# Optimization experiments

Hardware: AMD Instinct MI355X
Metric: run time of the kernel (lower is better)

Reference implementation:

```python
import jax, jax.numpy as jnp
import numpy as np

N, E, D, H, ED = 50000, 800000, 128, 4, 64
C = D // H  # per-head channels
EPS = 1e-5


def setup_inputs() -> dict:
    key = jax.random.key(0)
    ks = jax.random.split(key, 16)
    s = 0.05
    return {
        "x": jax.random.normal(ks[0], (N, D), jnp.float32),
        "edge_index": jax.random.randint(ks[1], (2, E), 0, N, jnp.int64 if jax.config.jax_enable_x64 else jnp.int32),
        "edge_attr": jax.random.normal(ks[2], (E, ED), jnp.float32),
        "Wq": jax.random.normal(ks[3], (D, H * C), jnp.float32) * s,
        "bq": jnp.zeros((H * C,), jnp.float32),
        "Wk": jax.random.normal(ks[4], (D, H * C), jnp.float32) * s,
        "bk": jnp.zeros((H * C,), jnp.float32),
        "Wv": jax.random.normal(ks[5], (D, H * C), jnp.float32) * s,
        "bv": jnp.zeros((H * C,), jnp.float32),
        "We": jax.random.normal(ks[6], (ED, H * C), jnp.float32) * s,  # lin_edge, bias=False
        "Wskip": jax.random.normal(ks[7], (D, H * C), jnp.float32) * s,
        "bskip": jnp.zeros((H * C,), jnp.float32),
        "Wbeta": jax.random.normal(ks[8], (3 * H * C, 1), jnp.float32) * s,  # lin_beta, bias=False
        "gamma": jnp.ones((D,), jnp.float32),
        "beta_ln": jnp.zeros((D,), jnp.float32),
    }


def _transformer_conv(x, src, dst, edge_attr, Wq, bq, Wk, bk, Wv, bv, We, Wskip, bskip, Wbeta):
    q = (x @ Wq + bq).reshape(N, H, C)
    k = (x @ Wk + bk).reshape(N, H, C)
    v = (x @ Wv + bv).reshape(N, H, C)
    e = (edge_attr @ We).reshape(E, H, C)
    k_j = k[src] + e                     # [E,H,C]
    v_j = v[src] + e                     # [E,H,C]
    alpha = jnp.einsum("ehc,ehc->eh", q[dst], k_j) / jnp.sqrt(jnp.float32(C))
    # per-destination softmax over incoming edges
    m = jax.ops.segment_max(alpha, dst, num_segments=N)          # [N,H]
    m = jnp.where(jnp.isfinite(m), m, 0.0)
    a = jnp.exp(alpha - m[dst])
    denom = jax.ops.segment_sum(a, dst, num_segments=N)          # [N,H]
    alpha = a / jnp.where(denom > 0, denom, 1.0)[dst]
    out = jax.ops.segment_sum(alpha[:, :, None] * v_j, dst, num_segments=N)  # [N,H,C]
    out = out.reshape(N, H * C)
    # beta-gated skip (beta=True, root_weight)
    x_r = x @ Wskip + bskip
    b = jax.nn.sigmoid(jnp.concatenate([out, x_r, out - x_r], axis=-1) @ Wbeta)  # [N,1]
    return b * x_r + (1.0 - b) * out


def reference(x, edge_index, edge_attr, Wq, bq, Wk, bk, Wv, bv, We, Wskip, bskip, Wbeta, gamma, beta_ln):
    src, dst = edge_index[0], edge_index[1]
    res = _transformer_conv(x, src, dst, edge_attr, Wq, bq, Wk, bk, Wv, bv, We, Wskip, bskip, Wbeta)
    out = jax.nn.gelu(res, approximate=False) + x
    mu = jnp.mean(out, axis=-1, keepdims=True)
    var = jnp.var(out, axis=-1, keepdims=True)
    return (out - mu) * jax.lax.rsqrt(var + EPS) * gamma + beta_ln
```

## Files before the change

### kernel.cpp

```cpp
#include <hip/hip_runtime.h>
#include <math.h>

#define NN 50000
#define EE 800000

typedef __bf16 bf16x8 __attribute__((ext_vector_type(8)));
typedef float f32x4 __attribute__((ext_vector_type(4)));
typedef float f32x2 __attribute__((ext_vector_type(2)));
typedef unsigned short ushort_t;
typedef unsigned int uint_t;

__device__ inline ushort_t f2bf(float f) {
  uint_t u = __float_as_uint(f);
  uint_t r = (u + 0x7fffu + ((u >> 16) & 1u)) >> 16;
  return (ushort_t)r;
}
__device__ inline float bflo(uint_t u) { return __uint_as_float(u << 16); }
__device__ inline float bfhi(uint_t u) { return __uint_as_float(u & 0xffff0000u); }

__device__ inline uint_t pk4_fp8(float a0, float a1, float a2, float a3) {
  a0 = fminf(fmaxf(a0, -448.f), 448.f);
  a1 = fminf(fmaxf(a1, -448.f), 448.f);
  a2 = fminf(fmaxf(a2, -448.f), 448.f);
  a3 = fminf(fmaxf(a3, -448.f), 448.f);
  uint_t lo = (uint_t)__builtin_amdgcn_cvt_pk_fp8_f32(a0, a1, 0, false) & 0xFFFFu;
  uint_t hi = (uint_t)__builtin_amdgcn_cvt_pk_fp8_f32(a2, a3, 0, false) & 0xFFFFu;
  return lo | (hi << 16);
}

__device__ inline void wave_sync() {
  asm volatile("s_waitcnt lgkmcnt(0)" ::: "memory");
  __builtin_amdgcn_wave_barrier();
}

__global__ __launch_bounds__(256) void k_prepA(const float* __restrict__ Wbeta,
                                               float* __restrict__ wcomb,
                                               int* __restrict__ counts) {
  int b = blockIdx.x;
  int o = threadIdx.x;
  if (b == 0) {
    if (o < 128) {
      wcomb[o]       = Wbeta[o]       + Wbeta[256 + o];
      wcomb[128 + o] = Wbeta[128 + o] - Wbeta[256 + o];
    }
  } else {
    int i = (b - 1) * 256 + o;
    if (i < NN) counts[i] = 0;
  }
}

__global__ __launch_bounds__(256) void k_prepB(
    const float* __restrict__ Wq, const float* __restrict__ Wk,
    const float* __restrict__ Wv, const float* __restrict__ Ws,
    const float* __restrict__ bq, const float* __restrict__ bk,
    const float* __restrict__ bv, const float* __restrict__ bs,
    ushort_t* __restrict__ Wbt, float* __restrict__ bcat,
    const float* __restrict__ We, ushort_t* __restrict__ WebT,
    const int* __restrict__ ei, int* __restrict__ counts) {
  int b = blockIdx.x;
  if (b >= 288) {
    int i = (b - 288) * 256 + threadIdx.x;
    if (i < EE) atomicAdd(&counts[ei[EE + i]], 1);
    return;
  }
  if (b >= 256) {
    int i = (b - 256) * 256 + threadIdx.x;
    int c = i >> 6, k = i & 63;
    WebT[c * 64 + k] = f2bf(We[k * 128 + c]);
    return;
  }
  int i = b * 256 + threadIdx.x;
  int c = i >> 7, k = i & 127;
  float w;
  if (c < 128)      w = Wq[k * 128 + c];
  else if (c < 256) w = Wk[k * 128 + (c - 128)];
  else if (c < 384) w = Wv[k * 128 + (c - 256)];
  else              w = Ws[k * 128 + (c - 384)];
  Wbt[(size_t)c * 128 + k] = f2bf(w);
  if (i < 512) {
    float bb;
    if (i < 128)      bb = bq[i];
    else if (i < 256) bb = bk[i - 128];
    else if (i < 384) bb = bv[i - 256];
    else              bb = bs[i - 384];
    bcat[i] = bb;
  }
}

__global__ __launch_bounds__(256) void k_mm(const float* __restrict__ x,
                                            const ushort_t* __restrict__ Wbt,
                                            const float* __restrict__ bcat,
                                            ushort_t* __restrict__ qb,
                                            ushort_t* __restrict__ kb,
                                            ushort_t* __restrict__ vb,
                                            ushort_t* __restrict__ xrb) {
  __shared__ ushort_t As[128 * 128];
  __shared__ ushort_t Bs[128 * 128];
  int t = threadIdx.x;
  int rb = blockIdx.x * 128;
  int cb = blockIdx.y * 128;

  for (int q = t; q < 2048; q += 256) {
    int r = q >> 4, j = q & 15;
    int row = rb + r;
    float4 f0 = make_float4(0.f, 0.f, 0.f, 0.f), f1 = f0;
    if (row < NN) {
      const float4* xp = (const float4*)&x[(size_t)row * 128 + j * 8];
      f0 = xp[0]; f1 = xp[1];
    }
    uint_t u0 = (uint_t)f2bf(f0.x) | ((uint_t)f2bf(f0.y) << 16);
    uint_t u1 = (uint_t)f2bf(f0.z) | ((uint_t)f2bf(f0.w) << 16);
    uint_t u2 = (uint_t)f2bf(f1.x) | ((uint_t)f2bf(f1.y) << 16);
    uint_t u3 = (uint_t)f2bf(f1.z) | ((uint_t)f2bf(f1.w) << 16);
    int e = r * 128 + ((j * 8) ^ ((r & 7) << 3));
    *(uint4*)&As[e] = make_uint4(u0, u1, u2, u3);
  }
  for (int q = t; q < 2048; q += 256) {
    int c = q >> 4, j = q & 15;
    uint4 w = *(const uint4*)&Wbt[(size_t)(cb + c) * 128 + j * 8];
    int e = c * 128 + ((j * 8) ^ ((c & 7) << 3));
    *(uint4*)&Bs[e] = w;
  }
  __syncthreads();

  int lane = t & 63;
  int wv = t >> 6;
  int wr = wv >> 1, wc = wv & 1;
  int l15 = lane & 15, l4 = lane >> 4;

  f32x4 acc[4][4];
#pragma unroll
  for (int i = 0; i < 4; ++i)
#pragma unroll
    for (int j = 0; j < 4; ++j) acc[i][j] = (f32x4){0.f, 0.f, 0.f, 0.f};

#pragma unroll
  for (int ks = 0; ks < 4; ++ks) {
    int kbv = ks * 32 + l4 * 8;
    bf16x8 af[4], bfr[4];
#pragma unroll
    for (int i = 0; i < 4; ++i) {
      int r = wr * 64 + i * 16 + l15;
      af[i] = *(const bf16x8*)&As[r * 128 + (kbv ^ ((r & 7) << 3))];
    }
#pragma unroll
    for (int j = 0; j < 4; ++j) {
      int c = wc * 64 + j * 16 + l15;
      bfr[j] = *(const bf16x8*)&Bs[c * 128 + (kbv ^ ((c & 7) << 3))];
    }
#pragma unroll
    for (int i = 0; i < 4; ++i)
#pragma unroll
      for (int j = 0; j < 4; ++j)
        acc[i][j] = __builtin_amdgcn_mfma_f32_16x16x32_bf16(af[i], bfr[j], acc[i][j], 0, 0, 0);
  }

  ushort_t* outp = (cb == 0) ? qb : (cb == 128) ? kb : (cb == 256) ? vb : xrb;
#pragma unroll
  for (int j = 0; j < 4; ++j) {
    int colg = wc * 64 + j * 16 + l15;
    float bv = bcat[cb + colg];
#pragma unroll
    for (int i = 0; i < 4; ++i) {
#pragma unroll
      for (int reg = 0; reg < 4; ++reg) {
        int grow = rb + wr * 64 + i * 16 + l4 * 4 + reg;
        if (grow < NN)
          outp[(size_t)grow * 128 + colg] = f2bf(acc[i][j][reg] + bv);
      }
    }
  }
}

__global__ __launch_bounds__(1024) void k_scan(int* __restrict__ counts, int* __restrict__ offsets) {
  __shared__ int wsum[16];
  __shared__ int s_carry;
  int4* counts4 = (int4*)counts;
  int4* offsets4 = (int4*)offsets;
  int t = threadIdx.x, lane = t & 63, w = t >> 6;
  if (t == 0) s_carry = 0;
  __syncthreads();
  for (int base = 0; base < 12500; base += 1024) {
    int idx = base + t;
    int4 v = (idx < 12500) ? counts4[idx] : make_int4(0, 0, 0, 0);
    int e1 = v.x, e2 = e1 + v.y, e3 = e2 + v.z, tot = e3 + v.w;
    int s = tot;
#pragma unroll
    for (int off = 1; off < 64; off <<= 1) {
      int u = __shfl_up(s, off);
      if (lane >= off) s += u;
    }
    if (lane == 63) wsum[w] = s;
    __syncthreads();
    if (t == 0) {
      int ex = s_carry;
#pragma unroll
      for (int i = 0; i < 16; ++i) { int tv = wsum[i]; wsum[i] = ex; ex += tv; }
      s_carry = ex;
    }
    __syncthreads();
    int be = wsum[w] + s - tot;
    if (idx < 12500) {
      int4 o = make_int4(be, be + e1, be + e2, be + e3);
      offsets4[idx] = o;
      counts4[idx] = o;
    }
    __syncthreads();
  }
  if (t == 0) offsets[NN] = s_carry;
}

__global__ __launch_bounds__(256) void k_fillw(const int* __restrict__ ei,
                                               int* __restrict__ cursors,
                                               const float* __restrict__ ea,
                                               const ushort_t* __restrict__ WebT,
                                               int* __restrict__ srcs,
                                               unsigned char* __restrict__ eaWperm) {
  __shared__ ushort_t As[64 * 64];
  __shared__ ushort_t Bs[128 * 64];
  __shared__ int sP[64];
  int t = threadIdx.x;
  int eb = blockIdx.x * 64;

  if (t < 64) {
    int e = eb + t;
    int d = ei[EE + e];
    int p = atomicAdd(&cursors[d], 1);
    sP[t] = p;
    srcs[p] = ei[e];
  }
  for (int q = t; q < 512; q += 256) {
    int r = q >> 3, j = q & 7;
    const float4* xp = (const float4*)&ea[(size_t)(eb + r) * 64 + j * 8];
    float4 f0 = xp[0], f1 = xp[1];
    uint_t u0 = (uint_t)f2bf(f0.x) | ((uint_t)f2bf(f0.y) << 16);
    uint_t u1 = (uint_t)f2bf(f0.z) | ((uint_t)f2bf(f0.w) << 16);
    uint_t u2 = (uint_t)f2bf(f1.x) | ((uint_t)f2bf(f1.y) << 16);
    uint_t u3 = (uint_t)f2bf(f1.z) | ((uint_t)f2bf(f1.w) << 16);
    *(uint4*)&As[r * 64 + ((j * 8) ^ ((r & 7) << 3))] = make_uint4(u0, u1, u2, u3);
  }
  for (int q = t; q < 1024; q += 256) {
    int c = q >> 3, j = q & 7;
    uint4 w = *(const uint4*)&WebT[(size_t)c * 64 + j * 8];
    *(uint4*)&Bs[c * 64 + ((j * 8) ^ ((c & 7) << 3))] = w;
  }
  __syncthreads();

  int lane = t & 63, wv = t >> 6;
  int l15 = lane & 15, l4 = lane >> 4;
  int edge = wv * 16 + l15;

  bf16x8 bfr[2];
#pragma unroll
  for (int ks = 0; ks < 2; ++ks) {
    int kbv = ks * 32 + l4 * 8;
    bfr[ks] = *(const bf16x8*)&As[edge * 64 + (kbv ^ ((edge & 7) << 3))];
  }

  f32x4 acc[8];
#pragma unroll
  for (int i = 0; i < 8; ++i) acc[i] = (f32x4){0.f, 0.f, 0.f, 0.f};

#pragma unroll
  for (int ks = 0; ks < 2; ++ks) {
    int kbv = ks * 32 + l4 * 8;
#pragma unroll
    for (int i = 0; i < 8; ++i) {
      int c = i * 16 + l15;
      bf16x8 af = *(const bf16x8*)&Bs[c * 64 + (kbv ^ ((c & 7) << 3))];
      acc[i] = __builtin_amdgcn_mfma_f32_16x16x32_bf16(af, bfr[ks], acc[i], 0, 0, 0);
    }
  }

  wave_sync();
  uint_t* dst32 = (uint_t*)As;
#pragma unroll
  for (int i = 0; i < 8; ++i)
    dst32[edge * 32 + ((i * 4 + l4) ^ ((edge & 7) << 2))] =
        pk4_fp8(acc[i][0], acc[i][1], acc[i][2], acc[i][3]);
  wave_sync();

  int el = wv * 16 + (lane >> 2), seg = lane & 3;
  int sw = (el & 7) << 2;
  const uint_t* src32 = (const uint_t*)As + el * 32;
  int w0 = (seg * 8) ^ sw;
  int w1 = (seg * 8 + 4) ^ sw;
  uint4 lo = *(const uint4*)&src32[w0];
  uint4 hi = *(const uint4*)&src32[w1];
  int p = sP[el];
  unsigned char* dst = eaWperm + (size_t)p * 128 + seg * 32;
  *(uint4*)dst = lo;
  *(uint4*)(dst + 16) = hi;
}

__global__ __launch_bounds__(256) void k_attn(
    const ushort_t* __restrict__ qb, const ushort_t* __restrict__ xrb,
    const ushort_t* __restrict__ kb, const ushort_t* __restrict__ vb,
    const unsigned char* __restrict__ eaWperm,
    const int* __restrict__ offsets, const int* __restrict__ srcs,
    const float* __restrict__ x, const float* __restrict__ wcomb,
    const float* __restrict__ gamma, const float* __restrict__ beta_ln,
    float* __restrict__ out) {
  __shared__ float sQ[4][128];
  __shared__ unsigned char sEA[4][16][144];
  __shared__ float sA[4][64];
  __shared__ int   sS[4][16];

  int t = threadIdx.x, wv = t >> 6, l = t & 63;
  int n = blockIdx.x * 4 + wv;
  int h = l >> 4, m = l & 15;
  int c0 = 2 * l, c1 = c0 + 1;
  const float scale = 0.17677669529663687f;

  uint_t qw = *(const uint_t*)&qb[(size_t)n * 128 + c0];
  *(float2*)&sQ[wv][c0] = make_float2(bflo(qw) * scale, bfhi(qw) * scale);
  if (l < 16) sS[wv][l] = 0;

  int js = offsets[n], je = offsets[n + 1];
  float acc0 = 0.f, acc1 = 0.f, lsum = 0.f;

  for (int base = js; base < je; base += 16) {
    int nj = je - base; if (nj > 16) nj = 16;
    wave_sync();

    uint4 e0 = {0,0,0,0}, e1 = {0,0,0,0};
    uint4 k0 = {0,0,0,0}, k1 = {0,0,0,0}, k2 = {0,0,0,0}, k3 = {0,0,0,0};
    if (m < nj) {
      int s = srcs[base + m];
      const uint4* erow = (const uint4*)(eaWperm + (size_t)(base + m) * 128 + 32 * h);
      e0 = erow[0]; e1 = erow[1];
      const uint4* krow = (const uint4*)(kb + (size_t)s * 128 + 32 * h);
      k0 = krow[0]; k1 = krow[1]; k2 = krow[2]; k3 = krow[3];
      if (h == 0) sS[wv][m] = s;
    }
    *(uint4*)&sEA[wv][m][32 * h]      = e0;
    *(uint4*)&sEA[wv][m][32 * h + 16] = e1;
    wave_sync();

    float z = 0.f;
    {
      const float* qp = &sQ[wv][32 * h];
      uint_t eu[8] = {e0.x, e0.y, e0.z, e0.w, e1.x, e1.y, e1.z, e1.w};
      uint_t ku[16] = {k0.x, k0.y, k0.z, k0.w, k1.x, k1.y, k1.z, k1.w,
                       k2.x, k2.y, k2.z, k2.w, k3.x, k3.y, k3.z, k3.w};
#pragma unroll
      for (int u = 0; u < 8; ++u) {
        f32x2 elo = __builtin_amdgcn_cvt_pk_f32_fp8(eu[u] & 0xFFFFu, false);
        f32x2 ehi = __builtin_amdgcn_cvt_pk_f32_fp8(eu[u] >> 16, false);
        float4 q4 = *(const float4*)&qp[4 * u];
        z += q4.x * (bflo(ku[2 * u]) + elo.x)
           + q4.y * (bfhi(ku[2 * u]) + elo.y)
           + q4.z * (bflo(ku[2 * u + 1]) + ehi.x)
           + q4.w * (bfhi(ku[2 * u + 1]) + ehi.y);
      }
    }
    float a = (m < nj) ? __expf(z) : 0.0f;
    lsum += a;
    sA[wv][l] = a;
    wave_sync();

    {
      int4 s0 = *(const int4*)&sS[wv][0];
      int4 s1 = *(const int4*)&sS[wv][4];
      f32x4 a0 = *(const f32x4*)&sA[wv][16 * h];
      f32x4 a1 = *(const f32x4*)&sA[wv][16 * h + 4];
      uint_t vv[8];
      int sidx[8] = {s0.x, s0.y, s0.z, s0.w, s1.x, s1.y, s1.z, s1.w};
#pragma unroll
      for (int e = 0; e < 8; ++e)
        vv[e] = *(const uint_t*)(vb + (size_t)sidx[e] * 128 + c0);
#pragma unroll
      for (int e = 0; e < 8; ++e) {
        float ae = (e < 4) ? a0[e] : a1[e - 4];
        uint_t ew = (uint_t)*(const ushort_t*)&sEA[wv][e][2 * l];
        f32x2 ef = __builtin_amdgcn_cvt_pk_f32_fp8(ew, false);
        acc0 += ae * (bflo(vv[e]) + ef.x);
        acc1 += ae * (bfhi(vv[e]) + ef.y);
      }
    }
    if (nj > 8) {
      int4 s2 = *(const int4*)&sS[wv][8];
      int4 s3 = *(const int4*)&sS[wv][12];
      f32x4 a2 = *(const f32x4*)&sA[wv][16 * h + 8];
      f32x4 a3 = *(const f32x4*)&sA[wv][16 * h + 12];
      uint_t vv[8];
      int sidx[8] = {s2.x, s2.y, s2.z, s2.w, s3.x, s3.y, s3.z, s3.w};
#pragma unroll
      for (int e = 0; e < 8; ++e)
        vv[e] = *(const uint_t*)(vb + (size_t)sidx[e] * 128 + c0);
#pragma unroll
      for (int e = 0; e < 8; ++e) {
        float ae = (e < 4) ? a2[e] : a3[e - 4];
        uint_t ew = (uint_t)*(const ushort_t*)&sEA[wv][8 + e][2 * l];
        f32x2 ef = __builtin_amdgcn_cvt_pk_f32_fp8(ew, false);
        acc0 += ae * (bflo(vv[e]) + ef.x);
        acc1 += ae * (bfhi(vv[e]) + ef.y);
      }
    }
  }

  lsum += __shfl_xor(lsum, 1); lsum += __shfl_xor(lsum, 2);
  lsum += __shfl_xor(lsum, 4); lsum += __shfl_xor(lsum, 8);

  float inv = (lsum > 0.f) ? (1.0f / lsum) : 1.0f;
  float o0 = acc0 * inv;
  float o1 = acc1 * inv;

  uint_t xw = *(const uint_t*)&xrb[(size_t)n * 128 + c0];
  float2 xrv = make_float2(bflo(xw), bfhi(xw));
  float bp = o0 * wcomb[c0] + o1 * wcomb[c1] + xrv.x * wcomb[128 + c0] + xrv.y * wcomb[128 + c1];
#pragma unroll
  for (int off = 32; off > 0; off >>= 1) bp += __shfl_xor(bp, off);
  float bgate = 1.0f / (1.0f + __expf(-bp));
  float r0 = bgate * xrv.x + (1.0f - bgate) * o0;
  float r1 = bgate * xrv.y + (1.0f - bgate) * o1;

  float2 xv = *(const float2*)&x[(size_t)n * 128 + c0];
  float ge0 = 0.5f * r0 * (1.0f + erff(r0 * 0.70710678118654752f)) + xv.x;
  float ge1 = 0.5f * r1 * (1.0f + erff(r1 * 0.70710678118654752f)) + xv.y;

  float s1 = ge0 + ge1;
  float s2 = ge0 * ge0 + ge1 * ge1;
#pragma unroll
  for (int off = 32; off > 0; off >>= 1) {
    s1 += __shfl_xor(s1, off);
    s2 += __shfl_xor(s2, off);
  }
  float mean = s1 * (1.0f / 128.0f);
  float var = s2 * (1.0f / 128.0f) - mean * mean;
  float rstd = rsqrtf(var + 1e-5f);
  float2 ov;
  ov.x = (ge0 - mean) * rstd * gamma[c0] + beta_ln[c0];
  ov.y = (ge1 - mean) * rstd * gamma[c1] + beta_ln[c1];
  *(float2*)&out[(size_t)n * 128 + c0] = ov;
}

extern "C" void kernel_launch(void* const* d_in, const int* in_sizes, int n_in,
                              void* d_out, int out_size, void* d_ws, size_t ws_size,
                              hipStream_t stream) {
  const float* x   = (const float*)d_in[0];
  const int*   ei  = (const int*)d_in[1];
  const float* ea  = (const float*)d_in[2];
  const float* Wq  = (const float*)d_in[3];
  const float* bq  = (const float*)d_in[4];
  const float* Wk  = (const float*)d_in[5];
  const float* bk  = (const float*)d_in[6];
  const float* Wv  = (const float*)d_in[7];
  const float* bv  = (const float*)d_in[8];
  const float* We  = (const float*)d_in[9];
  const float* Wsk = (const float*)d_in[10];
  const float* bsk = (const float*)d_in[11];
  const float* Wb  = (const float*)d_in[12];
  const float* gamma = (const float*)d_in[13];
  const float* beta  = (const float*)d_in[14];
  float* out = (float*)d_out;

  char* cur = (char*)d_ws;
  auto alloc = [&](size_t bytes) {
    void* p = (void*)cur;
    cur += (bytes + 255) & ~(size_t)255;
    return p;
  };
  ushort_t*      qbuf    = (ushort_t*)alloc((size_t)NN * 128 * 2);
  ushort_t*      kbuf    = (ushort_t*)alloc((size_t)NN * 128 * 2);
  ushort_t*      vbuf    = (ushort_t*)alloc((size_t)NN * 128 * 2);
  ushort_t*      xrbuf   = (ushort_t*)alloc((size_t)NN * 128 * 2);
  unsigned char* eaWperm = (unsigned char*)alloc((size_t)EE * 128);
  int*           srcs    = (int*)alloc((size_t)EE * 4);
  float*         wcomb   = (float*)alloc(256 * 4);
  float*         bcat    = (float*)alloc(512 * 4);
  ushort_t*      Wbt     = (ushort_t*)alloc((size_t)512 * 128 * 2);
  ushort_t*      WebT    = (ushort_t*)alloc((size_t)128 * 64 * 2);
  int*           counts  = (int*)alloc((size_t)NN * 4);
  int*           offsets = (int*)alloc((size_t)(NN + 4) * 4);

  k_prepA<<<197, 256, 0, stream>>>(Wb, wcomb, counts);
  k_prepB<<<288 + 3125, 256, 0, stream>>>(Wq, Wk, Wv, Wsk, bq, bk, bv, bsk,
                                          Wbt, bcat, We, WebT, ei, counts);
  k_mm<<<dim3(391, 4), 256, 0, stream>>>(x, Wbt, bcat, qbuf, kbuf, vbuf, xrbuf);
  k_scan<<<1, 1024, 0, stream>>>(counts, offsets);
  k_fillw<<<12500, 256, 0, stream>>>(ei, counts, ea, WebT, srcs, eaWperm);
  k_attn<<<12500, 256, 0, stream>>>(qbuf, xrbuf, kbuf, vbuf, eaWperm, offsets,
                                    srcs, x, wcomb, gamma, beta, out);
}
```

Before: 300.1 us.

## Prefetch next edge chunk in attention loop and fold scan into matmul launch

The attention kernel now software-pipelines its edge loop. It loads the next 16-edge chunk's source indices, edge features and K rows while the current chunk is being computed, and it issues all 16 V gathers before the dot products rather than after the softmax weights are known. Separately, the single-block prefix scan over destination counts now runs as an extra 256-thread block inside the matmul grid, which removes one kernel launch and lets the scan overlap the GEMM. The cost is higher register pressure in the attention kernel, which could lower occupancy. V rows are also now gathered even when a chunk holds eight or fewer edges; padded slots use source index zero, so the extra loads are wasted but safe.

```diff
diff --git a/kernel.cpp b/kernel.cpp
--- a/kernel.cpp
+++ b/kernel.cpp
@@ -87,16 +87,59 @@
   }
 }
 
-__global__ __launch_bounds__(256) void k_mm(const float* __restrict__ x,
-                                            const ushort_t* __restrict__ Wbt,
-                                            const float* __restrict__ bcat,
-                                            ushort_t* __restrict__ qb,
-                                            ushort_t* __restrict__ kb,
-                                            ushort_t* __restrict__ vb,
-                                            ushort_t* __restrict__ xrb) {
+__global__ __launch_bounds__(256) void k_mmscan(const float* __restrict__ x,
+                                                const ushort_t* __restrict__ Wbt,
+                                                const float* __restrict__ bcat,
+                                                ushort_t* __restrict__ qb,
+                                                ushort_t* __restrict__ kb,
+                                                ushort_t* __restrict__ vb,
+                                                ushort_t* __restrict__ xrb,
+                                                int* __restrict__ counts,
+                                                int* __restrict__ offsets) {
   __shared__ ushort_t As[128 * 128];
   __shared__ ushort_t Bs[128 * 128];
   int t = threadIdx.x;
+
+  if (blockIdx.x == 391) {
+    if (blockIdx.y != 0) return;
+    __shared__ int wsum[4];
+    __shared__ int s_carry;
+    int4* counts4 = (int4*)counts;
+    int4* offsets4 = (int4*)offsets;
+    int lane = t & 63, w = t >> 6;
+    if (t == 0) s_carry = 0;
+    __syncthreads();
+    for (int base = 0; base < 12500; base += 256) {
+      int idx = base + t;
+      int4 v = (idx < 12500) ? counts4[idx] : make_int4(0, 0, 0, 0);
+      int e1 = v.x, e2 = e1 + v.y, e3 = e2 + v.z, tot = e3 + v.w;
+      int s = tot;
+#pragma unroll
+      for (int off = 1; off < 64; off <<= 1) {
+        int u = __shfl_up(s, off);
+        if (lane >= off) s += u;
+      }
+      if (lane == 63) wsum[w] = s;
+      __syncthreads();
+      if (t == 0) {
+        int ex = s_carry;
+#pragma unroll
+        for (int i = 0; i < 4; ++i) { int tv = wsum[i]; wsum[i] = ex; ex += tv; }
+        s_carry = ex;
+      }
+      __syncthreads();
+      int be = wsum[w] + s - tot;
+      if (idx < 12500) {
+        int4 o = make_int4(be, be + e1, be + e2, be + e3);
+        offsets4[idx] = o;
+        counts4[idx] = o;
+      }
+      __syncthreads();
+    }
+    if (t == 0) offsets[NN] = s_carry;
+    return;
+  }
+
   int rb = blockIdx.x * 128;
   int cb = blockIdx.y * 128;
 
@@ -170,44 +213,6 @@
       }
     }
   }
-}
-
-__global__ __launch_bounds__(1024) void k_scan(int* __restrict__ counts, int* __restrict__ offsets) {
-  __shared__ int wsum[16];
-  __shared__ int s_carry;
-  int4* counts4 = (int4*)counts;
-  int4* offsets4 = (int4*)offsets;
-  int t = threadIdx.x, lane = t & 63, w = t >> 6;
-  if (t == 0) s_carry = 0;
-  __syncthreads();
-  for (int base = 0; base < 12500; base += 1024) {
-    int idx = base + t;
-    int4 v = (idx < 12500) ? counts4[idx] : make_int4(0, 0, 0, 0);
-    int e1 = v.x, e2 = e1 + v.y, e3 = e2 + v.z, tot = e3 + v.w;
-    int s = tot;
-#pragma unroll
-    for (int off = 1; off < 64; off <<= 1) {
-      int u = __shfl_up(s, off);
-      if (lane >= off) s += u;
-    }
-    if (lane == 63) wsum[w] = s;
-    __syncthreads();
-    if (t == 0) {
-      int ex = s_carry;
-#pragma unroll
-      for (int i = 0; i < 16; ++i) { int tv = wsum[i]; wsum[i] = ex; ex += tv; }
-      s_carry = ex;
-    }
-    __syncthreads();
-    int be = wsum[w] + s - tot;
-    if (idx < 12500) {
-      int4 o = make_int4(be, be + e1, be + e2, be + e3);
-      offsets4[idx] = o;
-      counts4[idx] = o;
-    }
-    __syncthreads();
-  }
-  if (t == 0) offsets[NN] = s_carry;
 }
 
 __global__ __launch_bounds__(256) void k_fillw(const int* __restrict__ ei,
@@ -319,23 +324,55 @@
   int js = offsets[n], je = offsets[n + 1];
   float acc0 = 0.f, acc1 = 0.f, lsum = 0.f;
 
+  uint4 e0 = {0,0,0,0}, e1 = {0,0,0,0};
+  uint4 k0 = {0,0,0,0}, k1 = {0,0,0,0}, k2 = {0,0,0,0}, k3 = {0,0,0,0};
+  int scur = 0;
+  if (m < je - js) {
+    scur = srcs[js + m];
+    const uint4* erow = (const uint4*)(eaWperm + (size_t)(js + m) * 128 + 32 * h);
+    e0 = erow[0]; e1 = erow[1];
+    const uint4* krow = (const uint4*)(kb + (size_t)scur * 128 + 32 * h);
+    k0 = krow[0]; k1 = krow[1]; k2 = krow[2]; k3 = krow[3];
+  }
+
   for (int base = js; base < je; base += 16) {
     int nj = je - base; if (nj > 16) nj = 16;
     wave_sync();
 
-    uint4 e0 = {0,0,0,0}, e1 = {0,0,0,0};
-    uint4 k0 = {0,0,0,0}, k1 = {0,0,0,0}, k2 = {0,0,0,0}, k3 = {0,0,0,0};
-    if (m < nj) {
-      int s = srcs[base + m];
-      const uint4* erow = (const uint4*)(eaWperm + (size_t)(base + m) * 128 + 32 * h);
-      e0 = erow[0]; e1 = erow[1];
-      const uint4* krow = (const uint4*)(kb + (size_t)s * 128 + 32 * h);
-      k0 = krow[0]; k1 = krow[1]; k2 = krow[2]; k3 = krow[3];
-      if (h == 0) sS[wv][m] = s;
-    }
     *(uint4*)&sEA[wv][m][32 * h]      = e0;
     *(uint4*)&sEA[wv][m][32 * h + 16] = e1;
+    if (h == 0) sS[wv][m] = scur;
+
+    uint4 ne0 = {0,0,0,0}, ne1 = {0,0,0,0};
+    uint4 nk0 = {0,0,0,0}, nk1 = {0,0,0,0}, nk2 = {0,0,0,0}, nk3 = {0,0,0,0};
+    int snx = 0;
+    int nb = base + 16;
+    if (nb < je && m < je - nb) {
+      snx = srcs[nb + m];
+      const uint4* erow = (const uint4*)(eaWperm + (size_t)(nb + m) * 128 + 32 * h);
+      ne0 = erow[0]; ne1 = erow[1];
+      const uint4* krow = (const uint4*)(kb + (size_t)snx * 128 + 32 * h);
+      nk0 = krow[0]; nk1 = krow[1]; nk2 = krow[2]; nk3 = krow[3];
+    }
     wave_sync();
+
+    int4 s0 = *(const int4*)&sS[wv][0];
+    int4 s1 = *(const int4*)&sS[wv][4];
+    int4 s2 = *(const int4*)&sS[wv][8];
+    int4 s3 = *(const int4*)&sS[wv][12];
+    uint_t vva[8], vvb[8];
+    {
+      int sidx[8] = {s0.x, s0.y, s0.z, s0.w, s1.x, s1.y, s1.z, s1.w};
+#pragma unroll
+      for (int e = 0; e < 8; ++e)
+        vva[e] = *(const uint_t*)(vb + (size_t)sidx[e] * 128 + c0);
+    }
+    {
+      int sidx[8] = {s2.x, s2.y, s2.z, s2.w, s3.x, s3.y, s3.z, s3.w};
+#pragma unroll
+      for (int e = 0; e < 8; ++e)
+        vvb[e] = *(const uint_t*)(vb + (size_t)sidx[e] * 128 + c0);
+    }
 
     float z = 0.f;
     {
@@ -360,43 +397,31 @@
     wave_sync();
 
     {
-      int4 s0 = *(const int4*)&sS[wv][0];
-      int4 s1 = *(const int4*)&sS[wv][4];
       f32x4 a0 = *(const f32x4*)&sA[wv][16 * h];
       f32x4 a1 = *(const f32x4*)&sA[wv][16 * h + 4];
-      uint_t vv[8];
-      int sidx[8] = {s0.x, s0.y, s0.z, s0.w, s1.x, s1.y, s1.z, s1.w};
-#pragma unroll
-      for (int e = 0; e < 8; ++e)
-        vv[e] = *(const uint_t*)(vb + (size_t)sidx[e] * 128 + c0);
 #pragma unroll
       for (int e = 0; e < 8; ++e) {
         float ae = (e < 4) ? a0[e] : a1[e - 4];
         uint_t ew = (uint_t)*(const ushort_t*)&sEA[wv][e][2 * l];
         f32x2 ef = __builtin_amdgcn_cvt_pk_f32_fp8(ew, false);
-        acc0 += ae * (bflo(vv[e]) + ef.x);
-        acc1 += ae * (bfhi(vv[e]) + ef.y);
+        acc0 += ae * (bflo(vva[e]) + ef.x);
+        acc1 += ae * (bfhi(vva[e]) + ef.y);
       }
     }
     if (nj > 8) {
-      int4 s2 = *(const int4*)&sS[wv][8];
-      int4 s3 = *(const int4*)&sS[wv][12];
       f32x4 a2 = *(const f32x4*)&sA[wv][16 * h + 8];
       f32x4 a3 = *(const f32x4*)&sA[wv][16 * h + 12];
-      uint_t vv[8];
-      int sidx[8] = {s2.x, s2.y, s2.z, s2.w, s3.x, s3.y, s3.z, s3.w};
-#pragma unroll
-      for (int e = 0; e < 8; ++e)
-        vv[e] = *(const uint_t*)(vb + (size_t)sidx[e] * 128 + c0);
 #pragma unroll
       for (int e = 0; e < 8; ++e) {
         float ae = (e < 4) ? a2[e] : a3[e - 4];
         uint_t ew = (uint_t)*(const ushort_t*)&sEA[wv][8 + e][2 * l];
         f32x2 ef = __builtin_amdgcn_cvt_pk_f32_fp8(ew, false);
-        acc0 += ae * (bflo(vv[e]) + ef.x);
-        acc1 += ae * (bfhi(vv[e]) + ef.y);
-      }
-    }
+        acc0 += ae * (bflo(vvb[e]) + ef.x);
+        acc1 += ae * (bfhi(vvb[e]) + ef.y);
+      }
+    }
+
+    e0 = ne0; e1 = ne1; k0 = nk0; k1 = nk1; k2 = nk2; k3 = nk3; scur = snx;
   }
 
   lsum += __shfl_xor(lsum, 1); lsum += __shfl_xor(lsum, 2);
@@ -477,8 +502,8 @@
   k_prepA<<<197, 256, 0, stream>>>(Wb, wcomb, counts);
   k_prepB<<<288 + 3125, 256, 0, stream>>>(Wq, Wk, Wv, Wsk, bq, bk, bv, bsk,
                                           Wbt, bcat, We, WebT, ei, counts);
-  k_mm<<<dim3(391, 4), 256, 0, stream>>>(x, Wbt, bcat, qbuf, kbuf, vbuf, xrbuf);
-  k_scan<<<1, 1024, 0, stream>>>(counts, offsets);
+  k_mmscan<<<dim3(392, 4), 256, 0, stream>>>(x, Wbt, bcat, qbuf, kbuf, vbuf,
+                                             xrbuf, counts, offsets);
   k_fillw<<<12500, 256, 0, stream>>>(ei, counts, ea, WebT, srcs, eaWperm);
   k_attn<<<12500, 256, 0, stream>>>(qbuf, xrbuf, kbuf, vbuf, eaWperm, offsets,
                                     srcs, x, wcomb, gamma, beta, out);
```

Result: faster. 292.8 us (-2.4%).
